# Kernel tuning notes

Measured on AMD Instinct MI355X. Metric: run time of the kernel, lower is better.

Reference implementation:

```python
import jax, jax.numpy as jnp
import numpy as np

B, N, D_IN, D_HID, N_ITER = 32, 512, 256, 128, 10


def setup_inputs() -> dict:
    key = jax.random.key(0)
    ks = jax.random.split(key, 8)
    s = 1.0 / np.sqrt(D_IN)  # torch Linear default init range
    return {
        "Xh": jax.random.normal(ks[0], (B, N, D_IN), jnp.float32),
        "Xm": jax.random.normal(ks[1], (B, N, D_IN), jnp.float32),
        # position 0 is the root; tokens 1..len are valid
        "lengths": jax.random.randint(ks[2], (B,), N // 2, N),
        "Wh": jax.random.uniform(ks[3], (D_HID, D_IN), jnp.float32, -s, s),
        "bh": jax.random.uniform(ks[4], (D_HID,), jnp.float32, -s, s),
        "Wm": jax.random.uniform(ks[5], (D_HID, D_IN), jnp.float32, -s, s),
        "bm": jax.random.uniform(ks[6], (D_HID,), jnp.float32, -s, s),
        "V": 0.01 * jax.random.normal(ks[7], (D_HID, D_HID), jnp.float32),
    }


def _logZ(scores, lengths):
    """Matrix-tree log-partition for single-root nonprojective trees.

    scores: [B,N,N] arc scores, scores[b,h,m] = head h -> modifier m, index 0 = root.
    lengths: [B] number of real tokens (valid modifiers at 1..len).
    """
    Bn, Nn, _ = scores.shape
    idx = jnp.arange(Nn)
    tok = (idx[None, :] >= 1) & (idx[None, :] <= lengths[:, None])   # [B,N] valid modifiers
    head = idx[None, :] <= lengths[:, None]                          # [B,N] valid heads (incl. root)
    pair = head[:, :, None] & tok[:, None, :] & (idx[:, None] != idx[None, :])
    # stability shift: every tree has exactly `len` edges, so logZ shifts by len*c
    c = jax.lax.stop_gradient(
        jnp.max(jnp.where(pair, scores, -jnp.inf), axis=(1, 2)))
    A = jnp.where(pair, jnp.exp(scores - c[:, None, None]), 0.0)     # [B,N,N]
    r = A[:, 0, 1:]                                                  # root -> token weights [B,N-1]
    At = A[:, 1:, 1:]                                                # token -> token weights
    ar = jnp.arange(Nn - 1)
    # Laplacian L = diag(colsum) - At (diag of At is zero by pair mask)
    Lap = (-At).at[:, ar, ar].set(r + At.sum(axis=1))
    # Koo et al. (2007): replace first row with root weights
    Lhat = Lap.at[:, 0, :].set(r)
    # padded positions: identity rows to keep det unchanged
    Lhat = Lhat.at[:, ar, ar].add(jnp.where(tok[:, 1:], 0.0, 1.0))
    _, logabs = jnp.linalg.slogdet(Lhat)
    return logabs + lengths.astype(scores.dtype) * c


def _marginals(scores, lengths):
    """nonprojective_marginals: (logZ, entropy, mu) via grad of logZ."""
    def f(s):
        lz = _logZ(s, lengths)
        return lz.sum(), lz
    (_, logZ), Y = jax.value_and_grad(f, has_aux=True)(scores)
    entr = logZ - jnp.sum(Y * scores, axis=(1, 2))
    return logZ, entr, Y


def reference(Xh, Xm, lengths, Wh, bh, Wm, bm, V):
    # dropout=0 -> H_mask/M_mask are ones
    H0 = Xh @ Wh.T + bh          # h_mlp(Xh), invariant across iterations
    M0 = Xm @ Wm.T + bm          # m_mlp(Xm)
    H = jax.nn.relu(H0)
    M = jax.nn.relu(M0)
    scores = jnp.einsum("bhu,uv,bmv->bhm", H, V, M)
    logZ, entr, Y = _marginals(scores, lengths)
    for _ in range(1, N_ITER):
        Hn = jax.nn.relu(H0 + Y @ M @ V.T)                       # _update_H
        Mn = jax.nn.relu(M0 + jnp.swapaxes(Y, -2, -1) @ H @ V)   # _update_M
        scores = jnp.einsum("bhu,uv,bmv->bhm", Hn, V, Mn)
        logZ, entr, Y = _marginals(scores, lengths)
        H, M = Hn, Mn
    return scores, logZ, Y, entr
```

## Files before the change

kernel.cpp:

```cpp
#include <hip/hip_runtime.h>
#include <math.h>

constexpr int BB = 32;
constexpr int NN_ = 512;
constexpr int DIN = 256;
constexpr int DH = 128;
constexpr int NITER = 10;
constexpr long HSTR = (long)NN_ * DH;
constexpr long SSTR = (long)NN_ * NN_;
constexpr long LSTR = 512L * 512L;

__device__ __forceinline__ unsigned f2mono(float f) {
    unsigned u = __float_as_uint(f);
    return (u & 0x80000000u) ? ~u : (u | 0x80000000u);
}
__device__ __forceinline__ float mono2f(unsigned u) {
    return __uint_as_float((u & 0x80000000u) ? (u & 0x7fffffffu) : ~u);
}

__device__ __forceinline__ float invert128(float r[8][8], int tid,
        float (*RowP)[8][132], float (*ColPT)[8][132], float (*Rnew)[8][132])
{
    int tx = tid & 15, ty = tid >> 4;
    int lane = tid & 63, w = tid >> 6;
    int li = lane >> 3, lj = lane & 7;
    const bool act = (tid < 256);
    float lacc = 0.f;
    __syncthreads();
    for (int s8 = 0; s8 < 16; ++s8) {
        int p = s8 & 1;
        if (act && ty == s8) {
            #pragma unroll
            for (int i = 0; i < 8; ++i)
                #pragma unroll
                for (int j = 0; j < 8; ++j)
                    RowP[p][i][tx * 8 + j] = r[i][j];
        }
        if (act && tx == s8) {
            float sub = (ty == s8) ? 1.f : 0.f;
            #pragma unroll
            for (int i = 0; i < 8; ++i)
                #pragma unroll
                for (int j = 0; j < 8; ++j)
                    ColPT[p][j][ty * 8 + i] = r[i][j] - ((i == j) ? sub : 0.f);
        }
        __syncthreads();
        float d = RowP[p][li][s8 * 8 + lj];
        float prod = 1.f;
        #pragma unroll
        for (int s = 0; s < 8; ++s) {
            float pv = __shfl(d, s * 9);
            prod *= pv;
            float pinv = 1.0f / pv;
            float rv = __shfl(d, s * 8 + lj);
            float cv = __shfl(d, li * 8 + s);
            float nd;
            if (li == s && lj == s)  nd = pinv;
            else if (li == s)        nd = rv * pinv;
            else if (lj == s)        nd = -cv * pinv;
            else                     nd = d - cv * pinv * rv;
            d = nd;
        }
        lacc += logf(fabsf(prod));
        if (act) {
            int sr = li;
            int jq = w * 32 + lj * 4;
            float dsr[8];
            #pragma unroll
            for (int t = 0; t < 8; ++t) dsr[t] = __shfl(d, (lane & 56) + t);
            float a0 = 0.f, a1 = 0.f, a2 = 0.f, a3 = 0.f;
            #pragma unroll
            for (int t = 0; t < 8; ++t) {
                float4 rp = *(const float4*)&RowP[p][t][jq];
                a0 += dsr[t] * rp.x; a1 += dsr[t] * rp.y;
                a2 += dsr[t] * rp.z; a3 += dsr[t] * rp.w;
            }
            if ((jq >> 3) == s8) {
                if ((jq & 7) == 0) {
                    a0 = dsr[0] + ((sr == 0) ? 1.f : 0.f);
                    a1 = dsr[1] + ((sr == 1) ? 1.f : 0.f);
                    a2 = dsr[2] + ((sr == 2) ? 1.f : 0.f);
                    a3 = dsr[3] + ((sr == 3) ? 1.f : 0.f);
                } else {
                    a0 = dsr[4] + ((sr == 4) ? 1.f : 0.f);
                    a1 = dsr[5] + ((sr == 5) ? 1.f : 0.f);
                    a2 = dsr[6] + ((sr == 6) ? 1.f : 0.f);
                    a3 = dsr[7] + ((sr == 7) ? 1.f : 0.f);
                }
            }
            *(float4*)&Rnew[p][sr][jq] = make_float4(a0, a1, a2, a3);
        }
        __syncthreads();
        if (act) {
            #pragma unroll
            for (int t = 0; t < 8; ++t) {
                float cp[8], rn[8];
                *(float4*)&cp[0] = *(const float4*)&ColPT[p][t][ty * 8];
                *(float4*)&cp[4] = *(const float4*)&ColPT[p][t][ty * 8 + 4];
                *(float4*)&rn[0] = *(const float4*)&Rnew[p][t][tx * 8];
                *(float4*)&rn[4] = *(const float4*)&Rnew[p][t][tx * 8 + 4];
                #pragma unroll
                for (int i = 0; i < 8; ++i)
                    #pragma unroll
                    for (int j = 0; j < 8; ++j)
                        r[i][j] -= cp[i] * rn[j];
            }
        }
    }
    return lacc;
}

template<int AMODE, int BMODE, int EPI>
__global__ __launch_bounds__(256) void gemm64(
    const float* __restrict__ A, const float* __restrict__ Bm,
    float* __restrict__ C, const float* __restrict__ Dp, float* __restrict__ C2,
    int Mdim, int Ndim, int Kdim,
    long sA, long sB, long sC, long sD)
{
    constexpr int BK = 16;
    __shared__ float As[BK][64 + 4];
    __shared__ float Bs[BK][64 + 4];
    int b = blockIdx.z;
    const float* Ab = A + (long)b * sA;
    const float* Bb = Bm + (long)b * sB;
    int m0 = blockIdx.x * 64, n0 = blockIdx.y * 64;
    int tid = threadIdx.x;
    int tx = tid & 15, ty = tid >> 4;
    float acc[4][4] = {};

    int arow, acol, brow, bcol;
    if (AMODE == 0) { arow = tid >> 2; acol = (tid & 3) * 4; }
    else            { arow = tid >> 4; acol = (tid & 15) * 4; }
    if (BMODE == 0) { brow = tid >> 4; bcol = (tid & 15) * 4; }
    else            { brow = tid >> 2; bcol = (tid & 3) * 4; }

    float4 av, bv;
    if (AMODE == 0) av = *(const float4*)(Ab + (long)(m0 + arow) * Kdim + acol);
    else            av = *(const float4*)(Ab + (long)(0 + arow) * Mdim + m0 + acol);
    if (BMODE == 0) bv = *(const float4*)(Bb + (long)(0 + brow) * Ndim + n0 + bcol);
    else            bv = *(const float4*)(Bb + (long)(n0 + brow) * Kdim + bcol);

    for (int k0 = 0; k0 < Kdim; k0 += BK) {
        __syncthreads();
        if (AMODE == 0) {
            As[acol + 0][arow] = av.x; As[acol + 1][arow] = av.y;
            As[acol + 2][arow] = av.z; As[acol + 3][arow] = av.w;
        } else {
            *(float4*)&As[arow][acol] = av;
        }
        if (BMODE == 0) {
            *(float4*)&Bs[brow][bcol] = bv;
        } else {
            Bs[bcol + 0][brow] = bv.x; Bs[bcol + 1][brow] = bv.y;
            Bs[bcol + 2][brow] = bv.z; Bs[bcol + 3][brow] = bv.w;
        }
        float4 av2, bv2;
        if (k0 + BK < Kdim) {
            int k1 = k0 + BK;
            if (AMODE == 0) av2 = *(const float4*)(Ab + (long)(m0 + arow) * Kdim + k1 + acol);
            else            av2 = *(const float4*)(Ab + (long)(k1 + arow) * Mdim + m0 + acol);
            if (BMODE == 0) bv2 = *(const float4*)(Bb + (long)(k1 + brow) * Ndim + n0 + bcol);
            else            bv2 = *(const float4*)(Bb + (long)(n0 + brow) * Kdim + k1 + bcol);
        }
        __syncthreads();
        #pragma unroll
        for (int k = 0; k < BK; ++k) {
            float4 a4 = *(const float4*)&As[k][ty * 4];
            float4 b4 = *(const float4*)&Bs[k][tx * 4];
            float avv[4] = {a4.x, a4.y, a4.z, a4.w};
            float bvv[4] = {b4.x, b4.y, b4.z, b4.w};
            #pragma unroll
            for (int i = 0; i < 4; ++i)
                #pragma unroll
                for (int j = 0; j < 4; ++j)
                    acc[i][j] += avv[i] * bvv[j];
        }
        av = av2; bv = bv2;
    }

    int r0 = m0 + ty * 4, c0 = n0 + tx * 4;
    if (EPI == 0) {
        float* Cb = C + (long)b * sC;
        #pragma unroll
        for (int i = 0; i < 4; ++i)
            *(float4*)(Cb + (long)(r0 + i) * Ndim + c0) =
                make_float4(acc[i][0], acc[i][1], acc[i][2], acc[i][3]);
    } else if (EPI == 1) {
        float4 bias = *(const float4*)(Dp + c0);
        float bb4[4] = {bias.x, bias.y, bias.z, bias.w};
        #pragma unroll
        for (int i = 0; i < 4; ++i) {
            float pre[4];
            #pragma unroll
            for (int j = 0; j < 4; ++j) pre[j] = acc[i][j] + bb4[j];
            *(float4*)(C2 + (long)(r0 + i) * Ndim + c0) =
                make_float4(pre[0], pre[1], pre[2], pre[3]);
            *(float4*)(C + (long)(r0 + i) * Ndim + c0) =
                make_float4(fmaxf(pre[0], 0.f), fmaxf(pre[1], 0.f),
                            fmaxf(pre[2], 0.f), fmaxf(pre[3], 0.f));
        }
    } else {
        const float* Db = Dp + (long)b * sD;
        float* Cb = C + (long)b * sC;
        #pragma unroll
        for (int i = 0; i < 4; ++i) {
            float4 d = *(const float4*)(Db + (long)(r0 + i) * Ndim + c0);
            float pre[4] = {acc[i][0] + d.x, acc[i][1] + d.y,
                            acc[i][2] + d.z, acc[i][3] + d.w};
            *(float4*)(Cb + (long)(r0 + i) * Ndim + c0) =
                make_float4(fmaxf(pre[0], 0.f), fmaxf(pre[1], 0.f),
                            fmaxf(pre[2], 0.f), fmaxf(pre[3], 0.f));
        }
    }
}

__global__ __launch_bounds__(256) void score_gemm(
    const float* __restrict__ A, const float* __restrict__ Bm,
    float* __restrict__ C, const int* __restrict__ len,
    unsigned* __restrict__ cu)
{
    int b = blockIdx.z;
    const float* Ab = A + (long)b * HSTR;
    const float* Bb = Bm + (long)b * HSTR;
    int m0 = blockIdx.x * 128, n0 = blockIdx.y * 128;
    int tid = threadIdx.x, tx = tid & 15, ty = tid >> 4;
    __shared__ float As[8][132];
    __shared__ float Bs[8][132];
    float acc[8][8] = {};
    int row = tid >> 1, kq = (tid & 1) << 2;
    float4 av = *(const float4*)(Ab + (long)(m0 + row) * DH + kq);
    float4 bv = *(const float4*)(Bb + (long)(n0 + row) * DH + kq);
    for (int kc = 0; kc < DH; kc += 8) {
        __syncthreads();
        As[kq + 0][row] = av.x; As[kq + 1][row] = av.y;
        As[kq + 2][row] = av.z; As[kq + 3][row] = av.w;
        Bs[kq + 0][row] = bv.x; Bs[kq + 1][row] = bv.y;
        Bs[kq + 2][row] = bv.z; Bs[kq + 3][row] = bv.w;
        float4 av2, bv2;
        if (kc + 8 < DH) {
            av2 = *(const float4*)(Ab + (long)(m0 + row) * DH + kc + 8 + kq);
            bv2 = *(const float4*)(Bb + (long)(n0 + row) * DH + kc + 8 + kq);
        }
        __syncthreads();
        #pragma unroll
        for (int k = 0; k < 8; ++k) {
            float a[8], bb[8];
            *(float4*)&a[0] = *(float4*)&As[k][ty * 8];
            *(float4*)&a[4] = *(float4*)&As[k][ty * 8 + 4];
            *(float4*)&bb[0] = *(float4*)&Bs[k][tx * 8];
            *(float4*)&bb[4] = *(float4*)&Bs[k][tx * 8 + 4];
            #pragma unroll
            for (int i = 0; i < 8; ++i)
                #pragma unroll
                for (int j = 0; j < 8; ++j) acc[i][j] += a[i] * bb[j];
        }
        av = av2; bv = bv2;
    }
    int L = len[b];
    float vmax = -3.0e38f;
    float* Cb = C + (long)b * SSTR;
    #pragma unroll
    for (int i = 0; i < 8; ++i) {
        int h = m0 + ty * 8 + i;
        bool hok = (h <= L);
        *(float4*)(Cb + (long)h * NN_ + n0 + tx * 8) =
            make_float4(acc[i][0], acc[i][1], acc[i][2], acc[i][3]);
        *(float4*)(Cb + (long)h * NN_ + n0 + tx * 8 + 4) =
            make_float4(acc[i][4], acc[i][5], acc[i][6], acc[i][7]);
        #pragma unroll
        for (int j = 0; j < 8; ++j) {
            int m = n0 + tx * 8 + j;
            if (hok && m >= 1 && m <= L && m != h) vmax = fmaxf(vmax, acc[i][j]);
        }
    }
    __syncthreads();
    float* red = &As[0][0];
    red[tid] = vmax; __syncthreads();
    for (int off = 128; off; off >>= 1) {
        if (tid < off) red[tid] = fmaxf(red[tid], red[tid + off]);
        __syncthreads();
    }
    if (tid == 0) atomicMax(&cu[b], f2mono(red[0]));
}

__global__ void zero_scal(float* scal) {
    if (threadIdx.x < 96) scal[threadIdx.x] = 0.f;
}

__global__ __launch_bounds__(256) void colsum_k(const float* __restrict__ sc,
                                                const int* __restrict__ len,
                                                const unsigned* __restrict__ cu,
                                                float* __restrict__ colsum)
{
    int b = blockIdx.x, yb = blockIdx.y;
    int tid = threadIdx.x, lane = tid & 63, w = tid >> 6;
    int L = len[b];
    float c = mono2f(cu[b]);
    int m = yb * 64 + lane;
    const float* S = sc + (long)b * SSTR;
    float s = 0.f;
    bool mv = (m >= 1 && m <= L);
    if (mv) {
        for (int h = 1 + w; h < NN_; h += 4) {
            if (h <= L && h != m) s += expf(S[(long)h * NN_ + m] - c);
        }
    }
    __shared__ float part[4][64];
    part[w][lane] = s; __syncthreads();
    if (tid < 64)
        colsum[(long)b * NN_ + yb * 64 + tid] =
            part[0][tid] + part[1][tid] + part[2][tid] + part[3][tid];
}

__global__ __launch_bounds__(256) void build_rows(const float* __restrict__ sc,
                                                  const int* __restrict__ len,
                                                  const unsigned* __restrict__ cu,
                                                  const float* __restrict__ colsum,
                                                  float* __restrict__ Lm,
                                                  float* __restrict__ Fb0,
                                                  float* __restrict__ logdet)
{
    __shared__ float sm[6][8][132];
    int b = blockIdx.x;
    int tid = threadIdx.x;
    int L = len[b];
    float c = mono2f(cu[b]);
    const float* S = sc + (long)b * SSTR;
    const float* cs = colsum + (long)b * NN_;

    if (blockIdx.y == 0) {
        int tx = tid & 15, ty = tid >> 4;
        float r[8][8];
        #pragma unroll
        for (int i = 0; i < 8; ++i) {
            int gi = ty * 8 + i;
            #pragma unroll
            for (int j = 0; j < 8; ++j) {
                int gj = tx * 8 + j;
                int tm = gj + 1;
                bool mv = (tm <= L);
                float v;
                if (gi == 0) {
                    v = mv ? expf(S[tm] - c) : 0.f;
                } else if (gi == gj) {
                    float rv = mv ? expf(S[tm] - c) : 0.f;
                    v = rv + cs[tm] + (mv ? 0.f : 1.f);
                } else {
                    int h = gi + 1;
                    v = (h <= L && mv) ? -expf(S[(long)h * NN_ + tm] - c) : 0.f;
                }
                r[i][j] = v;
            }
        }
        float lacc = invert128(r, tid,
                               (float(*)[8][132])&sm[0],
                               (float(*)[8][132])&sm[2],
                               (float(*)[8][132])&sm[4]);
        float* Ab = Lm + (long)b * LSTR;
        #pragma unroll
        for (int i = 0; i < 8; ++i) {
            *(float4*)(Ab + (long)(ty * 8 + i) * 512 + tx * 8) =
                make_float4(r[i][0], r[i][1], r[i][2], r[i][3]);
            *(float4*)(Ab + (long)(ty * 8 + i) * 512 + tx * 8 + 4) =
                make_float4(r[i][4], r[i][5], r[i][6], r[i][7]);
        }
        if (tid == 0) atomicAdd(&logdet[b], lacc);
        return;
    }

    int i0 = (blockIdx.y - 1) * 8;
    #pragma unroll
    for (int r = 0; r < 8; ++r) {
        int i = i0 + r;
        float* Lrow = Lm + (long)b * LSTR + (long)i * 512;
        float* Frow = Fb0 + (long)b * HSTR + (long)i * 128;
        #pragma unroll
        for (int q = 0; q < 2; ++q) {
            int j = tid + q * 256;
            float v;
            if (i == 511 || j == 511) {
                v = (i == j) ? 1.f : 0.f;
            } else {
                int tm = j + 1;
                bool mv = (tm <= L);
                if (i == 0) {
                    v = mv ? expf(S[tm] - c) : 0.f;
                } else if (i == j) {
                    float rv = mv ? expf(S[tm] - c) : 0.f;
                    v = rv + cs[tm] + ((tm > L) ? 1.f : 0.f);
                } else {
                    int h = i + 1;
                    v = (h <= L && mv) ? -expf(S[(long)h * NN_ + tm] - c) : 0.f;
                }
            }
            if (!(i < 128 && j < 128)) Lrow[j] = v;
            if (q == 0 && j < 128 && i >= 128) Frow[j] = v;
        }
    }
}

__global__ __launch_bounds__(256) void gj_panel(float* __restrict__ Lm,
                                                float* __restrict__ Fnext, int kb)
{
    int b = blockIdx.x, j = blockIdx.y;
    int jt = j + (j >= kb);
    int tid = threadIdx.x;
    float* base = Lm + (long)b * LSTR;
    const float* D = base + (long)(kb * 128) * 512 + kb * 128;
    float* Aj = base + (long)(kb * 128) * 512 + jt * 128;
    __shared__ float Ds_[8][132];
    __shared__ float Asj[8][132];
    int tx = tid & 15, ty = tid >> 4;
    int drow = tid >> 1, dkq = (tid & 1) << 2;
    int akr = tid >> 5, acq = (tid & 31) << 2;
    float acc[8][8] = {};
    float4 dv = *(const float4*)(D + (long)drow * 512 + dkq);
    float4 ajv = *(const float4*)(Aj + (long)akr * 512 + acq);
    for (int kc = 0; kc < 128; kc += 8) {
        __syncthreads();
        Ds_[dkq + 0][drow] = dv.x; Ds_[dkq + 1][drow] = dv.y;
        Ds_[dkq + 2][drow] = dv.z; Ds_[dkq + 3][drow] = dv.w;
        *(float4*)&Asj[akr][acq] = ajv;
        float4 dv2, ajv2;
        if (kc + 8 < 128) {
            dv2 = *(const float4*)(D + (long)drow * 512 + kc + 8 + dkq);
            ajv2 = *(const float4*)(Aj + (long)(kc + 8 + akr) * 512 + acq);
        }
        __syncthreads();
        #pragma unroll
        for (int k = 0; k < 8; ++k) {
            float a[8], bv[8];
            *(float4*)&a[0] = *(float4*)&Ds_[k][ty * 8];
            *(float4*)&a[4] = *(float4*)&Ds_[k][ty * 8 + 4];
            *(float4*)&bv[0] = *(float4*)&Asj[k][tx * 8];
            *(float4*)&bv[4] = *(float4*)&Asj[k][tx * 8 + 4];
            #pragma unroll
            for (int i = 0; i < 8; ++i)
                #pragma unroll
                for (int jj = 0; jj < 8; ++jj) acc[i][jj] += a[i] * bv[jj];
        }
        dv = dv2; ajv = ajv2;
    }
    bool dual = (jt == kb + 1);
    float* Fn = Fnext + (long)b * HSTR + (long)(kb * 128) * 128;
    #pragma unroll
    for (int i = 0; i < 8; ++i) {
        float4 o0 = make_float4(acc[i][0], acc[i][1], acc[i][2], acc[i][3]);
        float4 o1 = make_float4(acc[i][4], acc[i][5], acc[i][6], acc[i][7]);
        *(float4*)(Aj + (long)(ty * 8 + i) * 512 + tx * 8) = o0;
        *(float4*)(Aj + (long)(ty * 8 + i) * 512 + tx * 8 + 4) = o1;
        if (dual) {
            *(float4*)(Fn + (long)(ty * 8 + i) * 128 + tx * 8) = o0;
            *(float4*)(Fn + (long)(ty * 8 + i) * 128 + tx * 8 + 4) = o1;
        }
    }
}

__global__ __launch_bounds__(256) void gj_update64(
    float* __restrict__ Lm, const float* __restrict__ Fbuf,
    float* __restrict__ Fnext, int kb)
{
    constexpr int BK = 16;
    __shared__ float Fs[BK][68];
    __shared__ float Rs[BK][68];
    int b = blockIdx.x;
    int it = blockIdx.y;
    int ib = it + (it >= kb);
    int sub = blockIdx.z;
    int jt = sub >> 2;
    int quad = sub & 3;
    int r0 = (quad >> 1) * 64, c0 = (quad & 1) * 64;
    int tid = threadIdx.x;
    int tx = tid & 15, ty = tid >> 4;
    float* base = Lm + (long)b * LSTR;
    const float* F = Fbuf + (long)b * HSTR + (long)(ib * 128 + r0) * 128;
    const float* R = base + (long)(kb * 128) * 512 + jt * 128 + c0;
    float* Cb = base + (long)(ib * 128 + r0) * 512 + jt * 128 + c0;
    int frow = tid >> 2, fkq = (tid & 3) << 2;
    int rkr = tid >> 4, rcq = (tid & 15) << 2;
    float acc[4][4] = {};
    float4 fv = *(const float4*)(F + (long)frow * 128 + fkq);
    float4 rv = *(const float4*)(R + (long)rkr * 512 + rcq);
    for (int kc = 0; kc < 128; kc += BK) {
        __syncthreads();
        Fs[fkq + 0][frow] = fv.x; Fs[fkq + 1][frow] = fv.y;
        Fs[fkq + 2][frow] = fv.z; Fs[fkq + 3][frow] = fv.w;
        *(float4*)&Rs[rkr][rcq] = rv;
        float4 fv2, rv2;
        if (kc + BK < 128) {
            fv2 = *(const float4*)(F + (long)frow * 128 + kc + BK + fkq);
            rv2 = *(const float4*)(R + (long)(kc + BK + rkr) * 512 + rcq);
        }
        __syncthreads();
        #pragma unroll
        for (int k = 0; k < BK; ++k) {
            float4 a4 = *(const float4*)&Fs[k][ty * 4];
            float4 b4 = *(const float4*)&Rs[k][tx * 4];
            float a[4] = {a4.x, a4.y, a4.z, a4.w};
            float bb[4] = {b4.x, b4.y, b4.z, b4.w};
            #pragma unroll
            for (int i = 0; i < 4; ++i)
                #pragma unroll
                for (int j = 0; j < 4; ++j)
                    acc[i][j] += a[i] * bb[j];
        }
        fv = fv2; rv = rv2;
    }
    bool dual = (jt == kb + 1);
    float* Fn = Fnext + (long)b * HSTR + (long)(ib * 128 + r0) * 128 + c0;
    if (jt == kb) {
        #pragma unroll
        for (int i = 0; i < 4; ++i)
            *(float4*)(Cb + (long)(ty * 4 + i) * 512 + tx * 4) =
                make_float4(-acc[i][0], -acc[i][1], -acc[i][2], -acc[i][3]);
    } else {
        #pragma unroll
        for (int i = 0; i < 4; ++i) {
            float4 o = *(const float4*)(Cb + (long)(ty * 4 + i) * 512 + tx * 4);
            o = make_float4(o.x - acc[i][0], o.y - acc[i][1],
                            o.z - acc[i][2], o.w - acc[i][3]);
            *(float4*)(Cb + (long)(ty * 4 + i) * 512 + tx * 4) = o;
            if (dual) *(float4*)(Fn + (long)(ty * 4 + i) * 128 + tx * 4) = o;
        }
    }
}

__global__ __launch_bounds__(256) void inv_k(float* __restrict__ Lm,
                                             float* __restrict__ logdet, int kb)
{
    __shared__ float sm[6][8][132];
    int b = blockIdx.x;
    int tid = threadIdx.x;
    int tx = tid & 15, ty = tid >> 4;
    float* Dd = Lm + (long)b * LSTR + (long)(kb * 128) * 512 + kb * 128;
    float r[8][8];
    #pragma unroll
    for (int i = 0; i < 8; ++i) {
        *(float4*)&r[i][0] = *(const float4*)(Dd + (long)(ty * 8 + i) * 512 + tx * 8);
        *(float4*)&r[i][4] = *(const float4*)(Dd + (long)(ty * 8 + i) * 512 + tx * 8 + 4);
    }
    float lacc = invert128(r, tid,
                           (float(*)[8][132])&sm[0],
                           (float(*)[8][132])&sm[2],
                           (float(*)[8][132])&sm[4]);
    #pragma unroll
    for (int i = 0; i < 8; ++i) {
        *(float4*)(Dd + (long)(ty * 8 + i) * 512 + tx * 8) =
            make_float4(r[i][0], r[i][1], r[i][2], r[i][3]);
        *(float4*)(Dd + (long)(ty * 8 + i) * 512 + tx * 8 + 4) =
            make_float4(r[i][4], r[i][5], r[i][6], r[i][7]);
    }
    if (tid == 0) atomicAdd(&logdet[b], lacc);
}

__global__ __launch_bounds__(256) void y_k(const float* __restrict__ sc,
                                           const float* __restrict__ Binv,
                                           const int* __restrict__ len,
                                           const unsigned* __restrict__ cu,
                                           float* __restrict__ Y,
                                           float* __restrict__ Ssum)
{
    int b = blockIdx.x;
    int ht = blockIdx.y >> 3, mt = blockIdx.y & 7;
    int h0 = ht * 64, m0 = mt * 64;
    int tid = threadIdx.x;
    int L = len[b];
    float c = mono2f(cu[b]);
    const float* S = sc + (long)b * SSTR;
    const float* Bi = Binv + (long)b * LSTR;
    float* Yb = Y + (long)b * SSTR;
    __shared__ float Bs[64][65];
    __shared__ float Ds[64], C0s[64];
    {
        int hh = tid & 63, m4 = tid >> 6;
        int col = h0 + hh - 1;
        for (int mm = m4; mm < 64; mm += 4) {
            int row = m0 + mm - 1;
            Bs[mm][hh] = (row >= 0 && col >= 0) ? Bi[(long)row * 512 + col] : 0.f;
        }
    }
    if (tid < 64) {
        int row = m0 + tid - 1;
        Ds[tid] = (row >= 0) ? Bi[(long)row * 512 + row] : 0.f;
    } else if (tid < 128) {
        int mm = tid - 64, row = m0 + mm - 1;
        C0s[mm] = (row >= 0) ? Bi[(long)row * 512] : 0.f;
    }
    __syncthreads();
    int mm = tid & 63, hq = tid >> 6;
    int m = m0 + mm;
    float lsum = 0.f;
    bool mvalid = (m >= 1 && m <= L);
    float dterm = (m >= 2) ? Ds[mm] : 0.f;
    #pragma unroll
    for (int hi = 0; hi < 16; ++hi) {
        int hh = hq * 16 + hi;
        int h = h0 + hh;
        float s = S[(long)h * NN_ + m];
        float y = 0.f;
        if (mvalid && h <= L && h != m) {
            float a = expf(s - c);
            float g;
            if (h == 0) g = C0s[mm] + dterm;
            else g = dterm - ((h >= 2) ? Bs[mm][hh] : 0.f);
            y = a * g;
        }
        Yb[(long)h * NN_ + m] = y;
        lsum += y * s;
    }
    __shared__ float red[256];
    red[tid] = lsum; __syncthreads();
    for (int off = 128; off; off >>= 1) {
        if (tid < off) red[tid] += red[tid + off];
        __syncthreads();
    }
    if (tid == 0) atomicAdd(&Ssum[b], red[0]);
}

__global__ void fin_k(const int* __restrict__ len, unsigned* __restrict__ cu,
                      float* __restrict__ logdet, float* __restrict__ Ssum,
                      float* __restrict__ outLogZ, float* __restrict__ outEntr)
{
    int b = threadIdx.x;
    if (b < 32) {
        float c = mono2f(cu[b]);
        float lz = logdet[b] + (float)len[b] * c;
        outLogZ[b] = lz;
        outEntr[b] = lz - Ssum[b];
        cu[b] = 0u;
        logdet[b] = 0.f;
        Ssum[b] = 0.f;
    }
}

extern "C" void kernel_launch(void* const* d_in, const int* in_sizes, int n_in,
                              void* d_out, int out_size, void* d_ws, size_t ws_size,
                              hipStream_t stream)
{
    const float* Xh = (const float*)d_in[0];
    const float* Xm = (const float*)d_in[1];
    const int*   len = (const int*)d_in[2];
    const float* Wh = (const float*)d_in[3];
    const float* bh = (const float*)d_in[4];
    const float* Wm = (const float*)d_in[5];
    const float* bm = (const float*)d_in[6];
    const float* V  = (const float*)d_in[7];

    float* ws = (float*)d_ws;
    constexpr long U = 2097152;
    float* H0 = ws;
    float* M0 = ws + U;
    float* Ha = ws + 2 * U;
    float* Ma = ws + 3 * U;
    float* Hb = ws + 4 * U;
    float* Mb = ws + 5 * U;
    float* T1 = ws + 6 * U;
    float* Yt = ws + 7 * U;
    float* Lm = ws + 8 * U;
    float* cs = ws + 12 * U;
    float* scal = ws + 12 * U + 16384;
    unsigned* cu = (unsigned*)scal;
    float* logdet = scal + 32;
    float* Ssum = scal + 64;

    float* Sout = (float*)d_out;
    float* outLogZ = (float*)d_out + 8388608;
    float* Yout = (float*)d_out + 8388640;
    float* outEntr = (float*)d_out + 8388640 + 8388608;

    zero_scal<<<1, 96, 0, stream>>>(scal);

    gemm64<0,1,1><<<dim3(256, 2, 1), 256, 0, stream>>>(
        Xh, Wh, Ha, bh, H0, 16384, DH, DIN, 0, 0, 0, 0);
    gemm64<0,1,1><<<dim3(256, 2, 1), 256, 0, stream>>>(
        Xm, Wm, Ma, bm, M0, 16384, DH, DIN, 0, 0, 0, 0);

    float* Hc = Ha; float* Mc = Ma; float* Hn = Hb; float* Mn = Mb;
    for (int t = 0; t < NITER; ++t) {
        if (t > 0) {
            gemm64<0,1,0><<<dim3(8,2,BB),256,0,stream>>>(
                Mc, V, Yt, nullptr, nullptr, 512, DH, DH, HSTR, 0, HSTR, 0);
            gemm64<0,0,2><<<dim3(8,2,BB),256,0,stream>>>(
                Yout, Yt, Hn, H0, nullptr, 512, DH, 512, SSTR, HSTR, HSTR, HSTR);
            gemm64<1,0,2><<<dim3(8,2,BB),256,0,stream>>>(
                Yout, T1, Mn, M0, nullptr, 512, DH, 512, SSTR, HSTR, HSTR, HSTR);
            { float* tmp = Hc; Hc = Hn; Hn = tmp; }
            { float* tmp = Mc; Mc = Mn; Mn = tmp; }
        }
        gemm64<0,0,0><<<dim3(8,2,BB),256,0,stream>>>(
            Hc, V, T1, nullptr, nullptr, 512, DH, DH, HSTR, 0, HSTR, 0);
        score_gemm<<<dim3(4,4,BB),256,0,stream>>>(T1, Mc, Sout, len, cu);

        colsum_k<<<dim3(BB,8),256,0,stream>>>(Sout, len, cu, cs);
        build_rows<<<dim3(BB,65),256,0,stream>>>(Sout, len, cu, cs, Lm, Yt, logdet);

        float* Fbufs[2] = {Yt, Hn};
        for (int kb = 0; kb < 4; ++kb) {
            float* Fcur  = Fbufs[kb & 1];
            float* Fnext = Fbufs[(kb + 1) & 1];
            gj_panel<<<dim3(BB,3),256,0,stream>>>(Lm, Fnext, kb);
            gj_update64<<<dim3(BB,3,16),256,0,stream>>>(Lm, Fcur, Fnext, kb);
            if (kb < 3)
                inv_k<<<dim3(BB),256,0,stream>>>(Lm, logdet, kb + 1);
        }
        y_k<<<dim3(BB,64),256,0,stream>>>(Sout, Lm, len, cu, Yout, Ssum);
        fin_k<<<1,32,0,stream>>>(len, cu, logdet, Ssum, outLogZ, outEntr);
    }
}
```

Measured before the change: 5.793 ms.

## Fuse diagonal-block inversion into GJ update via atomic counters; split panel finer

Removes the separate inv_k launch per block step by folding it into gj_update64. An extra z-slice of blocks spins on a per-batch atomic counter until the four quadrant blocks that update the next diagonal tile have finished, then inverts it. Those quadrant blocks are remapped so they run first. gj_panel is also split into four 32-column sub-blocks with a 4x4 micro-tile to get more parallelism. The spin-wait depends on co-residency and dispatch order, and can deadlock if the waiting blocks take all CUs before the producer blocks are scheduled.

```diff
diff --git a/kernel.cpp b/kernel.cpp
--- a/kernel.cpp
+++ b/kernel.cpp
@@ -284,7 +284,7 @@
 }
 
 __global__ void zero_scal(float* scal) {
-    if (threadIdx.x < 96) scal[threadIdx.x] = 0.f;
+    if (threadIdx.x < 224) scal[threadIdx.x] = 0.f;
 }
 
 __global__ __launch_bounds__(256) void colsum_k(const float* __restrict__ sc,
@@ -402,75 +402,115 @@
 __global__ __launch_bounds__(256) void gj_panel(float* __restrict__ Lm,
                                                 float* __restrict__ Fnext, int kb)
 {
-    int b = blockIdx.x, j = blockIdx.y;
+    constexpr int BK = 16;
+    __shared__ float Ds[BK][132];
+    __shared__ float As2[BK][36];
+    int b = blockIdx.x;
+    int j = blockIdx.y >> 2;
+    int cq = blockIdx.y & 3;
     int jt = j + (j >= kb);
+    int c0 = cq * 32;
     int tid = threadIdx.x;
+    int tx = tid & 7, ty = tid >> 3;
     float* base = Lm + (long)b * LSTR;
     const float* D = base + (long)(kb * 128) * 512 + kb * 128;
     float* Aj = base + (long)(kb * 128) * 512 + jt * 128;
-    __shared__ float Ds_[8][132];
-    __shared__ float Asj[8][132];
-    int tx = tid & 15, ty = tid >> 4;
-    int drow = tid >> 1, dkq = (tid & 1) << 2;
-    int akr = tid >> 5, acq = (tid & 31) << 2;
-    float acc[8][8] = {};
-    float4 dv = *(const float4*)(D + (long)drow * 512 + dkq);
-    float4 ajv = *(const float4*)(Aj + (long)akr * 512 + acq);
-    for (int kc = 0; kc < 128; kc += 8) {
-        __syncthreads();
-        Ds_[dkq + 0][drow] = dv.x; Ds_[dkq + 1][drow] = dv.y;
-        Ds_[dkq + 2][drow] = dv.z; Ds_[dkq + 3][drow] = dv.w;
-        *(float4*)&Asj[akr][acq] = ajv;
-        float4 dv2, ajv2;
-        if (kc + 8 < 128) {
-            dv2 = *(const float4*)(D + (long)drow * 512 + kc + 8 + dkq);
-            ajv2 = *(const float4*)(Aj + (long)(kc + 8 + akr) * 512 + acq);
-        }
-        __syncthreads();
-        #pragma unroll
-        for (int k = 0; k < 8; ++k) {
-            float a[8], bv[8];
-            *(float4*)&a[0] = *(float4*)&Ds_[k][ty * 8];
-            *(float4*)&a[4] = *(float4*)&Ds_[k][ty * 8 + 4];
-            *(float4*)&bv[0] = *(float4*)&Asj[k][tx * 8];
-            *(float4*)&bv[4] = *(float4*)&Asj[k][tx * 8 + 4];
-            #pragma unroll
-            for (int i = 0; i < 8; ++i)
+    int drow = tid >> 1, dk8 = (tid & 1) * 8;
+    int akr = tid >> 3, acq4 = (tid & 7) * 4;
+    bool aload = (akr < BK);
+    float acc[4][4] = {};
+    float4 dva = *(const float4*)(D + (long)drow * 512 + dk8);
+    float4 dvb = *(const float4*)(D + (long)drow * 512 + dk8 + 4);
+    float4 av;
+    if (aload) av = *(const float4*)(Aj + (long)akr * 512 + c0 + acq4);
+    for (int kc = 0; kc < 128; kc += BK) {
+        __syncthreads();
+        Ds[dk8 + 0][drow] = dva.x; Ds[dk8 + 1][drow] = dva.y;
+        Ds[dk8 + 2][drow] = dva.z; Ds[dk8 + 3][drow] = dva.w;
+        Ds[dk8 + 4][drow] = dvb.x; Ds[dk8 + 5][drow] = dvb.y;
+        Ds[dk8 + 6][drow] = dvb.z; Ds[dk8 + 7][drow] = dvb.w;
+        if (aload) *(float4*)&As2[akr][acq4] = av;
+        float4 dva2, dvb2, av2;
+        if (kc + BK < 128) {
+            dva2 = *(const float4*)(D + (long)drow * 512 + kc + BK + dk8);
+            dvb2 = *(const float4*)(D + (long)drow * 512 + kc + BK + dk8 + 4);
+            if (aload) av2 = *(const float4*)(Aj + (long)(kc + BK + akr) * 512 + c0 + acq4);
+        }
+        __syncthreads();
+        #pragma unroll
+        for (int k = 0; k < BK; ++k) {
+            float4 a4 = *(const float4*)&Ds[k][ty * 4];
+            float4 b4 = *(const float4*)&As2[k][tx * 4];
+            float a[4] = {a4.x, a4.y, a4.z, a4.w};
+            float bb[4] = {b4.x, b4.y, b4.z, b4.w};
+            #pragma unroll
+            for (int i = 0; i < 4; ++i)
                 #pragma unroll
-                for (int jj = 0; jj < 8; ++jj) acc[i][jj] += a[i] * bv[jj];
-        }
-        dv = dv2; ajv = ajv2;
+                for (int jj = 0; jj < 4; ++jj)
+                    acc[i][jj] += a[i] * bb[jj];
+        }
+        dva = dva2; dvb = dvb2; av = av2;
     }
     bool dual = (jt == kb + 1);
     float* Fn = Fnext + (long)b * HSTR + (long)(kb * 128) * 128;
     #pragma unroll
-    for (int i = 0; i < 8; ++i) {
-        float4 o0 = make_float4(acc[i][0], acc[i][1], acc[i][2], acc[i][3]);
-        float4 o1 = make_float4(acc[i][4], acc[i][5], acc[i][6], acc[i][7]);
-        *(float4*)(Aj + (long)(ty * 8 + i) * 512 + tx * 8) = o0;
-        *(float4*)(Aj + (long)(ty * 8 + i) * 512 + tx * 8 + 4) = o1;
-        if (dual) {
-            *(float4*)(Fn + (long)(ty * 8 + i) * 128 + tx * 8) = o0;
-            *(float4*)(Fn + (long)(ty * 8 + i) * 128 + tx * 8 + 4) = o1;
-        }
+    for (int i = 0; i < 4; ++i) {
+        float4 o = make_float4(acc[i][0], acc[i][1], acc[i][2], acc[i][3]);
+        *(float4*)(Aj + (long)(ty * 4 + i) * 512 + c0 + tx * 4) = o;
+        if (dual) *(float4*)(Fn + (long)(ty * 4 + i) * 128 + c0 + tx * 4) = o;
     }
 }
 
 __global__ __launch_bounds__(256) void gj_update64(
     float* __restrict__ Lm, const float* __restrict__ Fbuf,
-    float* __restrict__ Fnext, int kb)
+    float* __restrict__ Fnext, float* __restrict__ logdet,
+    unsigned* __restrict__ cnt, int kb)
 {
     constexpr int BK = 16;
-    __shared__ float Fs[BK][68];
-    __shared__ float Rs[BK][68];
+    __shared__ float sm[6 * 8 * 132];
     int b = blockIdx.x;
-    int it = blockIdx.y;
+    int tid = threadIdx.x;
+
+    if (blockIdx.z == 0) {
+        if (blockIdx.y != 0 || kb >= 3) return;
+        if (tid == 0) {
+            while (__hip_atomic_load(&cnt[kb * 32 + b], __ATOMIC_ACQUIRE,
+                                     __HIP_MEMORY_SCOPE_AGENT) < 4u) {}
+        }
+        __syncthreads();
+        int tx = tid & 15, ty = tid >> 4;
+        float* Dd = Lm + (long)b * LSTR + (long)((kb + 1) * 128) * 512 + (kb + 1) * 128;
+        float r[8][8];
+        #pragma unroll
+        for (int i = 0; i < 8; ++i) {
+            *(float4*)&r[i][0] = *(const float4*)(Dd + (long)(ty * 8 + i) * 512 + tx * 8);
+            *(float4*)&r[i][4] = *(const float4*)(Dd + (long)(ty * 8 + i) * 512 + tx * 8 + 4);
+        }
+        float lacc = invert128(r, tid,
+                               (float(*)[8][132])sm,
+                               (float(*)[8][132])(sm + 2 * 8 * 132),
+                               (float(*)[8][132])(sm + 4 * 8 * 132));
+        #pragma unroll
+        for (int i = 0; i < 8; ++i) {
+            *(float4*)(Dd + (long)(ty * 8 + i) * 512 + tx * 8) =
+                make_float4(r[i][0], r[i][1], r[i][2], r[i][3]);
+            *(float4*)(Dd + (long)(ty * 8 + i) * 512 + tx * 8 + 4) =
+                make_float4(r[i][4], r[i][5], r[i][6], r[i][7]);
+        }
+        if (tid == 0) atomicAdd(&logdet[b], lacc);
+        return;
+    }
+
+    float (*Fs)[68] = (float (*)[68])sm;
+    float (*Rs)[68] = (float (*)[68])(sm + BK * 68);
+    int il = blockIdx.y;
+    int it = (kb < 3) ? ((il == 0) ? kb : (il == kb ? 0 : il)) : il;
     int ib = it + (it >= kb);
-    int sub = blockIdx.z;
-    int jt = sub >> 2;
+    int sub = blockIdx.z - 1;
+    int jl = sub >> 2;
+    int jt = (kb < 3) ? ((jl == 0) ? kb + 1 : (jl == kb + 1 ? 0 : jl)) : jl;
     int quad = sub & 3;
     int r0 = (quad >> 1) * 64, c0 = (quad & 1) * 64;
-    int tid = threadIdx.x;
     int tx = tid & 15, ty = tid >> 4;
     float* base = Lm + (long)b * LSTR;
     const float* F = Fbuf + (long)b * HSTR + (long)(ib * 128 + r0) * 128;
@@ -523,34 +563,13 @@
             if (dual) *(float4*)(Fn + (long)(ty * 4 + i) * 128 + tx * 4) = o;
         }
     }
-}
-
-__global__ __launch_bounds__(256) void inv_k(float* __restrict__ Lm,
-                                             float* __restrict__ logdet, int kb)
-{
-    __shared__ float sm[6][8][132];
-    int b = blockIdx.x;
-    int tid = threadIdx.x;
-    int tx = tid & 15, ty = tid >> 4;
-    float* Dd = Lm + (long)b * LSTR + (long)(kb * 128) * 512 + kb * 128;
-    float r[8][8];
-    #pragma unroll
-    for (int i = 0; i < 8; ++i) {
-        *(float4*)&r[i][0] = *(const float4*)(Dd + (long)(ty * 8 + i) * 512 + tx * 8);
-        *(float4*)&r[i][4] = *(const float4*)(Dd + (long)(ty * 8 + i) * 512 + tx * 8 + 4);
-    }
-    float lacc = invert128(r, tid,
-                           (float(*)[8][132])&sm[0],
-                           (float(*)[8][132])&sm[2],
-                           (float(*)[8][132])&sm[4]);
-    #pragma unroll
-    for (int i = 0; i < 8; ++i) {
-        *(float4*)(Dd + (long)(ty * 8 + i) * 512 + tx * 8) =
-            make_float4(r[i][0], r[i][1], r[i][2], r[i][3]);
-        *(float4*)(Dd + (long)(ty * 8 + i) * 512 + tx * 8 + 4) =
-            make_float4(r[i][4], r[i][5], r[i][6], r[i][7]);
-    }
-    if (tid == 0) atomicAdd(&logdet[b], lacc);
+    if (kb < 3 && ib == kb + 1 && jt == kb + 1) {
+        __threadfence();
+        __syncthreads();
+        if (tid == 0)
+            __hip_atomic_fetch_add(&cnt[kb * 32 + b], 1u, __ATOMIC_RELEASE,
+                                   __HIP_MEMORY_SCOPE_AGENT);
+    }
 }
 
 __global__ __launch_bounds__(256) void y_k(const float* __restrict__ sc,
@@ -619,6 +638,7 @@
 
 __global__ void fin_k(const int* __restrict__ len, unsigned* __restrict__ cu,
                       float* __restrict__ logdet, float* __restrict__ Ssum,
+                      unsigned* __restrict__ cnt,
                       float* __restrict__ outLogZ, float* __restrict__ outEntr)
 {
     int b = threadIdx.x;
@@ -630,6 +650,10 @@
         cu[b] = 0u;
         logdet[b] = 0.f;
         Ssum[b] = 0.f;
+        cnt[b] = 0u;
+        cnt[32 + b] = 0u;
+        cnt[64 + b] = 0u;
+        cnt[96 + b] = 0u;
     }
 }
 
@@ -662,13 +686,14 @@
     unsigned* cu = (unsigned*)scal;
     float* logdet = scal + 32;
     float* Ssum = scal + 64;
+    unsigned* cnt = (unsigned*)(scal + 96);
 
     float* Sout = (float*)d_out;
     float* outLogZ = (float*)d_out + 8388608;
     float* Yout = (float*)d_out + 8388640;
     float* outEntr = (float*)d_out + 8388640 + 8388608;
 
-    zero_scal<<<1, 96, 0, stream>>>(scal);
+    zero_scal<<<1, 256, 0, stream>>>(scal);
 
     gemm64<0,1,1><<<dim3(256, 2, 1), 256, 0, stream>>>(
         Xh, Wh, Ha, bh, H0, 16384, DH, DIN, 0, 0, 0, 0);
@@ -698,12 +723,10 @@
         for (int kb = 0; kb < 4; ++kb) {
             float* Fcur  = Fbufs[kb & 1];
             float* Fnext = Fbufs[(kb + 1) & 1];
-            gj_panel<<<dim3(BB,3),256,0,stream>>>(Lm, Fnext, kb);
-            gj_update64<<<dim3(BB,3,16),256,0,stream>>>(Lm, Fcur, Fnext, kb);
-            if (kb < 3)
-                inv_k<<<dim3(BB),256,0,stream>>>(Lm, logdet, kb + 1);
+            gj_panel<<<dim3(BB,12),256,0,stream>>>(Lm, Fnext, kb);
+            gj_update64<<<dim3(BB,3,17),256,0,stream>>>(Lm, Fcur, Fnext, logdet, cnt, kb);
         }
         y_k<<<dim3(BB,64),256,0,stream>>>(Sout, Lm, len, cu, Yout, Ssum);
-        fin_k<<<1,32,0,stream>>>(len, cu, logdet, Ssum, outLogZ, outEntr);
-    }
-}
+        fin_k<<<1,32,0,stream>>>(len, cu, logdet, Ssum, cnt, outLogZ, outEntr);
+    }
+}
```

Result: no change. 5.861 ms (+1.2%).
